# Kernel tuning notes

Hardware: AMD Instinct MI355X
Metric: run time of the kernel (lower is better)

## Reference

```python
import jax, jax.numpy as jnp
import numpy as np

N = 125000   # lattice cells (50^3)
K = 26       # max neighbors (3D Moore neighborhood)
D = 32       # state_size
STEPS = 3    # CNF integration steps (explicit Euler)


def setup_inputs() -> dict:
    key = jax.random.key(0)
    ks = jax.random.split(key, 12)
    s = 0.1  # small init so tanh stays in its linear-ish regime
    return {
        "full_lattice_states": jax.random.normal(ks[0], (N, D), jnp.float32),
        "neighbor_indices": jax.random.randint(ks[1], (N, K), 0, N, jnp.int32),
        "tier_ids": jax.random.randint(ks[2], (N, K), 0, 3, jnp.int32),
        # local expert (SimpleLinear): [cur ; local_agg] -> D
        "W_loc": jax.random.normal(ks[3], (2 * D, D), jnp.float32) * s,
        "b_loc": jnp.zeros((D,), jnp.float32),
        # functional expert (HybridGNN): per-neighbor message + combine
        "W_msg": jax.random.normal(ks[4], (D, D), jnp.float32) * s,
        "b_msg": jnp.zeros((D,), jnp.float32),
        "W_fun": jax.random.normal(ks[5], (2 * D, D), jnp.float32) * s,
        "b_fun": jnp.zeros((D,), jnp.float32),
        # distant expert (LightweightCNF): ODE drift on [x ; distant_agg]
        "W_cnf": jax.random.normal(ks[6], (2 * D, D), jnp.float32) * s,
        "b_cnf": jnp.zeros((D,), jnp.float32),
        # gating network: [cur ; local_agg ; func_agg ; dist_agg] -> 3 experts
        "W_gate": jax.random.normal(ks[7], (4 * D, 3), jnp.float32) * s,
        "b_gate": jnp.zeros((3,), jnp.float32),
    }


def reference(full_lattice_states, neighbor_indices, tier_ids,
              W_loc, b_loc, W_msg, b_msg, W_fun, b_fun,
              W_cnf, b_cnf, W_gate, b_gate):
    cur = full_lattice_states                      # [N, D]
    nbr = full_lattice_states[neighbor_indices]    # [N, K, D] gather (irregular access)

    def tier_mean(x, t):
        # masked mean over neighbors belonging to tier t
        m = (tier_ids == t)[..., None].astype(x.dtype)           # [N, K, 1]
        return (x * m).sum(axis=1) / jnp.maximum(m.sum(axis=1), 1.0)  # [N, D]

    local_agg = tier_mean(nbr, 0)   # [N, D]
    func_agg = tier_mean(nbr, 1)    # [N, D]
    dist_agg = tier_mean(nbr, 2)    # [N, D]

    # local expert: single linear on [cur ; local_agg]
    local_out = jnp.tanh(jnp.concatenate([cur, local_agg], -1) @ W_loc + b_loc)

    # functional expert: GNN message passing over functional-tier neighbors
    msgs = jnp.tanh(nbr @ W_msg + b_msg)           # [N, K, D]
    func_msg = tier_mean(msgs, 1)                  # [N, D]
    func_out = jnp.tanh(jnp.concatenate([cur, func_msg], -1) @ W_fun + b_fun)

    # distant expert: lightweight CNF, explicit Euler conditioned on dist_agg
    dt = 1.0 / STEPS
    x = cur
    for _ in range(STEPS):
        x = x + dt * jnp.tanh(jnp.concatenate([x, dist_agg], -1) @ W_cnf + b_cnf)
    dist_out = x

    # gating: adaptive weighting of the 3 experts
    gate_in = jnp.concatenate([cur, local_agg, func_agg, dist_agg], -1)  # [N, 4D]
    w = jax.nn.softmax(gate_in @ W_gate + b_gate, axis=-1)               # [N, 3]

    out = (w[:, 0:1] * local_out + w[:, 1:2] * func_out + w[:, 2:3] * dist_out)
    return out
```

## Files before the change

kernel.cpp:

```cpp
#include <hip/hip_runtime.h>
#include <hip/hip_bf16.h>
#include <math.h>

#define NCELL 125000
#define KNBR  26
#define D     32
#define MC    64

#define SXE (127.0f/7.0f)
#define SXD (7.0f/127.0f)
#define SMD (1.0f/127.0f)

typedef unsigned int uint4v __attribute__((ext_vector_type(4)));
typedef float float4v __attribute__((ext_vector_type(4)));

__device__ __forceinline__ float fast_tanh(float x) {
    float e = __expf(2.0f * x);
    return 1.0f - 2.0f / (e + 1.0f);
}
__device__ __forceinline__ float bf2f(unsigned int h) {
    return __uint_as_float(h << 16);
}
__device__ __forceinline__ unsigned short f2bf(float f) {
    unsigned int u = __float_as_uint(f);
    u += 0x7fffu + ((u >> 16) & 1u);
    return (unsigned short)(u >> 16);
}

__global__ void __launch_bounds__(256) msg_kernel(
    const float* __restrict__ X, const float* __restrict__ Wm,
    const float* __restrict__ bm, unsigned short* __restrict__ XM)
{
    __shared__ float sX[256];
    int t = blockIdx.x * 256 + threadIdx.x;
    float v = X[t];
    sX[threadIdx.x] = v;
    __syncthreads();
    int d = t & 31;
    int base = threadIdx.x & ~31;
    float acc = bm[d];
#pragma unroll
    for (int j = 0; j < D; ++j)
        acc = fmaf(sX[base + j], Wm[j * D + d], acc);
    int xq = __float2int_rn(fminf(fmaxf(v, -7.f), 7.f) * SXE);
    int mq = __float2int_rn(fast_tanh(acc) * 127.0f);
    XM[t] = (unsigned short)(((mq & 0xff) << 8) | (xq & 0xff));
}

__global__ void __launch_bounds__(256) agg_kernel(
    const unsigned short* __restrict__ XM,
    const int* __restrict__ nbr, const int* __restrict__ tier,
    unsigned short* __restrict__ aggs)
{
    __shared__ int sPack[8 * KNBR];
    int tid = threadIdx.x;
    int blockCell = blockIdx.x * 8;
    if (tid < 8 * KNBR) {
        int g = blockCell * KNBR + tid;
        int jj = __builtin_nontemporal_load(&nbr[g]);
        int tt = __builtin_nontemporal_load(&tier[g]);
        sPack[tid] = (jj << 2) | tt;
    }
    __syncthreads();

    int grp = tid >> 5, d = tid & 31;
    int c = blockCell + grp;
    int sAll = 0, s0 = 0, s1 = 0, sm = 0, n0 = 0, n1 = 0;
#pragma unroll
    for (int k = 0; k < KNBR; ++k) {
        int pk = sPack[grp * KNBR + k];
        int tt = pk & 3;
        int j  = pk >> 2;
        unsigned short v = XM[j * D + d];
        int x = (int)(signed char)(v & 0xff);
        int m = (int)(signed char)(v >> 8);
        bool t0 = (tt == 0), t1 = (tt == 1);
        sAll += x;
        s0 += t0 ? x : 0;   n0 += t0;
        s1 += t1 ? x : 0;   n1 += t1;
        sm += t1 ? m : 0;
    }
    int s2 = sAll - s0 - s1;
    float n2 = (float)(KNBR - n0 - n1);
    unsigned short* a = aggs + (size_t)c * 4 * D + d;
    __builtin_nontemporal_store(f2bf((float)s0 * SXD / fmaxf((float)n0, 1.f)), a + 0 * D);
    __builtin_nontemporal_store(f2bf((float)s1 * SXD / fmaxf((float)n1, 1.f)), a + 1 * D);
    __builtin_nontemporal_store(f2bf((float)s2 * SXD / fmaxf(n2, 1.f)),        a + 2 * D);
    __builtin_nontemporal_store(f2bf((float)sm * SMD / fmaxf((float)n1, 1.f)), a + 3 * D);
}

__global__ void __launch_bounds__(256) moe_kernel(
    const float* __restrict__ X, const unsigned int* __restrict__ aggs,
    const float* __restrict__ Wl, const float* __restrict__ bl,
    const float* __restrict__ Wf, const float* __restrict__ bfv,
    const float* __restrict__ Wc, const float* __restrict__ bc,
    const float* __restrict__ Wg, const float* __restrict__ bg,
    float* __restrict__ out)
{
    __shared__ float sX[MC * 32];
    __shared__ unsigned int sA[MC * 64];
    int tid  = threadIdx.x;
    int base = blockIdx.x * MC;
    int cells = NCELL - base; if (cells > MC) cells = MC;

    const float4* gX = (const float4*)(X + (size_t)base * 32);
#pragma unroll
    for (int k = 0; k < 2; ++k) {
        int q4 = tid + k * 256;
        if (q4 * 4 < cells * 32) {
            float4 v = gX[q4];
            int g = q4 * 4, cc = g >> 5, j = g & 31, s = cc & 31;
            sX[cc * 32 + ((j + 0) ^ s)] = v.x;
            sX[cc * 32 + ((j + 1) ^ s)] = v.y;
            sX[cc * 32 + ((j + 2) ^ s)] = v.z;
            sX[cc * 32 + ((j + 3) ^ s)] = v.w;
        }
    }
    const uint4v* gA = (const uint4v*)(aggs + (size_t)base * 64);
#pragma unroll
    for (int k = 0; k < 4; ++k) {
        int q4 = tid + k * 256;
        if (q4 * 4 < cells * 64) {
            uint4v v = __builtin_nontemporal_load(&gA[q4]);
            int g = q4 * 4, cc = g >> 6, p = g & 63, s = cc & 31;
            sA[cc * 64 + ((p + 0) ^ s)] = v.x;
            sA[cc * 64 + ((p + 1) ^ s)] = v.y;
            sA[cc * 64 + ((p + 2) ^ s)] = v.z;
            sA[cc * 64 + ((p + 3) ^ s)] = v.w;
        }
    }
    __syncthreads();

    int role = tid >> 6, cc = tid & 63;
    int s = cc & 31;
    bool act = (cc < cells);
    float res[32];
    float w0 = 0.f, w1 = 0.f, w2 = 0.f;

    if (act && role == 0) {
        float g0 = bg[0], g1 = bg[1], g2 = bg[2];
#pragma unroll 8
        for (int j = 0; j < 32; ++j) {
            float v = sX[cc * 32 + (j ^ s)];
            g0 = fmaf(v, Wg[j*3+0], g0); g1 = fmaf(v, Wg[j*3+1], g1); g2 = fmaf(v, Wg[j*3+2], g2);
        }
#pragma unroll 8
        for (int p = 0; p < 48; ++p) {
            unsigned int dw = sA[cc * 64 + (p ^ s)];
            float vlo = bf2f(dw & 0xffffu), vhi = bf2f(dw >> 16);
            int r = 32 + p * 2;
            g0 = fmaf(vlo, Wg[r*3+0], g0); g1 = fmaf(vlo, Wg[r*3+1], g1); g2 = fmaf(vlo, Wg[r*3+2], g2);
            g0 = fmaf(vhi, Wg[(r+1)*3+0], g0); g1 = fmaf(vhi, Wg[(r+1)*3+1], g1); g2 = fmaf(vhi, Wg[(r+1)*3+2], g2);
        }
        float mx = fmaxf(g0, fmaxf(g1, g2));
        float e0 = __expf(g0 - mx), e1 = __expf(g1 - mx), e2 = __expf(g2 - mx);
        float inv = 1.f / (e0 + e1 + e2);
        w0 = e0 * inv; w1 = e1 * inv; w2 = e2 * inv;
    } else if (act && role == 1) {
        float gc[32], xx[32];
#pragma unroll
        for (int d0 = 0; d0 < 32; ++d0) gc[d0] = bc[d0];
#pragma unroll 4
        for (int p = 0; p < 16; ++p) {
            unsigned int dw = sA[cc * 64 + ((32 + p) ^ s)];
            float vlo = bf2f(dw & 0xffffu), vhi = bf2f(dw >> 16);
            int j = 32 + p * 2;
#pragma unroll
            for (int d0 = 0; d0 < 32; ++d0) gc[d0] = fmaf(vlo, Wc[j * 32 + d0], gc[d0]);
#pragma unroll
            for (int d0 = 0; d0 < 32; ++d0) gc[d0] = fmaf(vhi, Wc[(j + 1) * 32 + d0], gc[d0]);
        }
#pragma unroll
        for (int d0 = 0; d0 < 32; ++d0) xx[d0] = sX[cc * 32 + (d0 ^ s)];
        const float dt = 1.0f / 3.0f;
#pragma unroll 1
        for (int st = 0; st < 3; ++st) {
#pragma unroll
            for (int d0 = 0; d0 < 32; ++d0) res[d0] = gc[d0];
#pragma unroll 8
            for (int j = 0; j < 32; ++j) {
                float v = xx[j];
#pragma unroll
                for (int d0 = 0; d0 < 32; ++d0) res[d0] = fmaf(v, Wc[j * 32 + d0], res[d0]);
            }
#pragma unroll
            for (int d0 = 0; d0 < 32; ++d0) xx[d0] += dt * fast_tanh(res[d0]);
        }
#pragma unroll
        for (int d0 = 0; d0 < 32; ++d0) res[d0] = xx[d0];
    } else if (act && role == 2) {
#pragma unroll
        for (int d0 = 0; d0 < 32; ++d0) res[d0] = bl[d0];
#pragma unroll 8
        for (int j = 0; j < 32; ++j) {
            float v = sX[cc * 32 + (j ^ s)];
#pragma unroll
            for (int d0 = 0; d0 < 32; ++d0) res[d0] = fmaf(v, Wl[j * 32 + d0], res[d0]);
        }
#pragma unroll 4
        for (int p = 0; p < 16; ++p) {
            unsigned int dw = sA[cc * 64 + (p ^ s)];
            float vlo = bf2f(dw & 0xffffu), vhi = bf2f(dw >> 16);
            int j = 32 + p * 2;
#pragma unroll
            for (int d0 = 0; d0 < 32; ++d0) res[d0] = fmaf(vlo, Wl[j * 32 + d0], res[d0]);
#pragma unroll
            for (int d0 = 0; d0 < 32; ++d0) res[d0] = fmaf(vhi, Wl[(j + 1) * 32 + d0], res[d0]);
        }
#pragma unroll
        for (int d0 = 0; d0 < 32; ++d0) res[d0] = fast_tanh(res[d0]);
    } else if (act && role == 3) {
#pragma unroll
        for (int d0 = 0; d0 < 32; ++d0) res[d0] = bfv[d0];
#pragma unroll 8
        for (int j = 0; j < 32; ++j) {
            float v = sX[cc * 32 + (j ^ s)];
#pragma unroll
            for (int d0 = 0; d0 < 32; ++d0) res[d0] = fmaf(v, Wf[j * 32 + d0], res[d0]);
        }
#pragma unroll 4
        for (int p = 0; p < 16; ++p) {
            unsigned int dw = sA[cc * 64 + ((48 + p) ^ s)];
            float vlo = bf2f(dw & 0xffffu), vhi = bf2f(dw >> 16);
            int j = 32 + p * 2;
#pragma unroll
            for (int d0 = 0; d0 < 32; ++d0) res[d0] = fmaf(vlo, Wf[j * 32 + d0], res[d0]);
#pragma unroll
            for (int d0 = 0; d0 < 32; ++d0) res[d0] = fmaf(vhi, Wf[(j + 1) * 32 + d0], res[d0]);
        }
#pragma unroll
        for (int d0 = 0; d0 < 32; ++d0) res[d0] = fast_tanh(res[d0]);
    }
    __syncthreads();

    float* sFr = (float*)sA;
    float* sCr = sFr + MC * 32;
    if (act) {
        if (role == 2) {
#pragma unroll
            for (int d0 = 0; d0 < 32; ++d0) sX[cc * 32 + (d0 ^ s)] = res[d0];
        } else if (role == 3) {
#pragma unroll
            for (int d0 = 0; d0 < 32; ++d0) sFr[cc * 32 + (d0 ^ s)] = res[d0];
        } else if (role == 1) {
#pragma unroll
            for (int d0 = 0; d0 < 32; ++d0) sCr[cc * 32 + (d0 ^ s)] = res[d0];
        }
    }
    __syncthreads();

    if (act && role == 0) {
        float o[32];
#pragma unroll
        for (int d0 = 0; d0 < 32; ++d0) {
            float lo = sX [cc * 32 + (d0 ^ s)];
            float fo = sFr[cc * 32 + (d0 ^ s)];
            float xo = sCr[cc * 32 + (d0 ^ s)];
            o[d0] = w0 * lo + w1 * fo + w2 * xo;
        }
#pragma unroll
        for (int d0 = 0; d0 < 32; ++d0) sX[cc * 32 + (d0 ^ s)] = o[d0];
    }
    __syncthreads();

    float4v* gO = (float4v*)(out + (size_t)base * 32);
#pragma unroll
    for (int k = 0; k < 2; ++k) {
        int q4 = tid + k * 256;
        if (q4 * 4 < cells * 32) {
            int g = q4 * 4, cc2 = g >> 5, j = g & 31, s2 = cc2 & 31;
            float4v v;
            v.x = sX[cc2 * 32 + ((j + 0) ^ s2)];
            v.y = sX[cc2 * 32 + ((j + 1) ^ s2)];
            v.z = sX[cc2 * 32 + ((j + 2) ^ s2)];
            v.w = sX[cc2 * 32 + ((j + 3) ^ s2)];
            __builtin_nontemporal_store(v, &gO[q4]);
        }
    }
}

extern "C" void kernel_launch(void* const* d_in, const int* in_sizes, int n_in,
                              void* d_out, int out_size, void* d_ws, size_t ws_size,
                              hipStream_t stream)
{
    const float* X    = (const float*)d_in[0];
    const int*   nbr  = (const int*)  d_in[1];
    const int*   tier = (const int*)  d_in[2];
    const float* Wl   = (const float*)d_in[3];
    const float* bl   = (const float*)d_in[4];
    const float* Wm   = (const float*)d_in[5];
    const float* bm   = (const float*)d_in[6];
    const float* Wf   = (const float*)d_in[7];
    const float* bf   = (const float*)d_in[8];
    const float* Wc   = (const float*)d_in[9];
    const float* bc   = (const float*)d_in[10];
    const float* Wg   = (const float*)d_in[11];
    const float* bg   = (const float*)d_in[12];
    float* out = (float*)d_out;

    const size_t ND = (size_t)NCELL * D;
    unsigned short* XM = (unsigned short*)d_ws;
    unsigned short* aggs = XM + ND;

    dim3 blk(256);
    msg_kernel<<<dim3(ND / 256), blk, 0, stream>>>(X, Wm, bm, XM);
    agg_kernel<<<dim3(NCELL / 8), blk, 0, stream>>>(XM, nbr, tier, aggs);
    moe_kernel<<<dim3((NCELL + MC - 1) / MC), blk, 0, stream>>>(
        X, (const unsigned int*)aggs, Wl, bl, Wf, bf, Wc, bc, Wg, bg, out);
}
```

Before: 226.5 us.

## Fuse neighbor aggregation into MoE kernel via shared-memory aggregates

```diff
diff --git a/kernel.cpp b/kernel.cpp
--- a/kernel.cpp
+++ b/kernel.cpp
@@ -11,7 +11,6 @@
 #define SXD (7.0f/127.0f)
 #define SMD (1.0f/127.0f)
 
-typedef unsigned int uint4v __attribute__((ext_vector_type(4)));
 typedef float float4v __attribute__((ext_vector_type(4)));
 
 __device__ __forceinline__ float fast_tanh(float x) {
@@ -47,50 +46,9 @@
     XM[t] = (unsigned short)(((mq & 0xff) << 8) | (xq & 0xff));
 }
 
-__global__ void __launch_bounds__(256) agg_kernel(
-    const unsigned short* __restrict__ XM,
+__global__ void __launch_bounds__(256) fused_kernel(
+    const float* __restrict__ X, const unsigned short* __restrict__ XM,
     const int* __restrict__ nbr, const int* __restrict__ tier,
-    unsigned short* __restrict__ aggs)
-{
-    __shared__ int sPack[8 * KNBR];
-    int tid = threadIdx.x;
-    int blockCell = blockIdx.x * 8;
-    if (tid < 8 * KNBR) {
-        int g = blockCell * KNBR + tid;
-        int jj = __builtin_nontemporal_load(&nbr[g]);
-        int tt = __builtin_nontemporal_load(&tier[g]);
-        sPack[tid] = (jj << 2) | tt;
-    }
-    __syncthreads();
-
-    int grp = tid >> 5, d = tid & 31;
-    int c = blockCell + grp;
-    int sAll = 0, s0 = 0, s1 = 0, sm = 0, n0 = 0, n1 = 0;
-#pragma unroll
-    for (int k = 0; k < KNBR; ++k) {
-        int pk = sPack[grp * KNBR + k];
-        int tt = pk & 3;
-        int j  = pk >> 2;
-        unsigned short v = XM[j * D + d];
-        int x = (int)(signed char)(v & 0xff);
-        int m = (int)(signed char)(v >> 8);
-        bool t0 = (tt == 0), t1 = (tt == 1);
-        sAll += x;
-        s0 += t0 ? x : 0;   n0 += t0;
-        s1 += t1 ? x : 0;   n1 += t1;
-        sm += t1 ? m : 0;
-    }
-    int s2 = sAll - s0 - s1;
-    float n2 = (float)(KNBR - n0 - n1);
-    unsigned short* a = aggs + (size_t)c * 4 * D + d;
-    __builtin_nontemporal_store(f2bf((float)s0 * SXD / fmaxf((float)n0, 1.f)), a + 0 * D);
-    __builtin_nontemporal_store(f2bf((float)s1 * SXD / fmaxf((float)n1, 1.f)), a + 1 * D);
-    __builtin_nontemporal_store(f2bf((float)s2 * SXD / fmaxf(n2, 1.f)),        a + 2 * D);
-    __builtin_nontemporal_store(f2bf((float)sm * SMD / fmaxf((float)n1, 1.f)), a + 3 * D);
-}
-
-__global__ void __launch_bounds__(256) moe_kernel(
-    const float* __restrict__ X, const unsigned int* __restrict__ aggs,
     const float* __restrict__ Wl, const float* __restrict__ bl,
     const float* __restrict__ Wf, const float* __restrict__ bfv,
     const float* __restrict__ Wc, const float* __restrict__ bc,
@@ -99,10 +57,18 @@
 {
     __shared__ float sX[MC * 32];
     __shared__ unsigned int sA[MC * 64];
+    __shared__ int sPack[MC * KNBR];
+    unsigned short* sA16 = (unsigned short*)sA;
+
     int tid  = threadIdx.x;
     int base = blockIdx.x * MC;
     int cells = NCELL - base; if (cells > MC) cells = MC;
 
+    for (int i = tid; i < cells * KNBR; i += 256) {
+        int jj = __builtin_nontemporal_load(&nbr[base * KNBR + i]);
+        int tt = __builtin_nontemporal_load(&tier[base * KNBR + i]);
+        sPack[i] = (jj << 2) | tt;
+    }
     const float4* gX = (const float4*)(X + (size_t)base * 32);
 #pragma unroll
     for (int k = 0; k < 2; ++k) {
@@ -116,17 +82,36 @@
             sX[cc * 32 + ((j + 3) ^ s)] = v.w;
         }
     }
-    const uint4v* gA = (const uint4v*)(aggs + (size_t)base * 64);
-#pragma unroll
-    for (int k = 0; k < 4; ++k) {
-        int q4 = tid + k * 256;
-        if (q4 * 4 < cells * 64) {
-            uint4v v = __builtin_nontemporal_load(&gA[q4]);
-            int g = q4 * 4, cc = g >> 6, p = g & 63, s = cc & 31;
-            sA[cc * 64 + ((p + 0) ^ s)] = v.x;
-            sA[cc * 64 + ((p + 1) ^ s)] = v.y;
-            sA[cc * 64 + ((p + 2) ^ s)] = v.z;
-            sA[cc * 64 + ((p + 3) ^ s)] = v.w;
+    __syncthreads();
+
+    int grp = tid >> 5, d = tid & 31;
+#pragma unroll 1
+    for (int slot = grp; slot < MC; slot += 8) {
+        if (slot < cells) {
+            int sAll = 0, s0 = 0, s1 = 0, sm = 0, n0 = 0, n1 = 0;
+#pragma unroll
+            for (int k = 0; k < KNBR; ++k) {
+                int pk = sPack[slot * KNBR + k];
+                int tt = pk & 3;
+                int j  = pk >> 2;
+                unsigned short v = XM[j * D + d];
+                int x = (int)(signed char)(v & 0xff);
+                int m = (int)(signed char)(v >> 8);
+                bool t0 = (tt == 0), t1 = (tt == 1);
+                sAll += x;
+                s0 += t0 ? x : 0;   n0 += t0;
+                s1 += t1 ? x : 0;   n1 += t1;
+                sm += t1 ? m : 0;
+            }
+            int s2 = sAll - s0 - s1;
+            float n2 = (float)(KNBR - n0 - n1);
+            int s = slot & 31;
+            int b16 = slot * 128;
+            int p = d >> 1, h = d & 1;
+            sA16[b16 + ((( 0 + p) ^ s) << 1) + h] = f2bf((float)s0 * SXD / fmaxf((float)n0, 1.f));
+            sA16[b16 + (((16 + p) ^ s) << 1) + h] = f2bf((float)s1 * SXD / fmaxf((float)n1, 1.f));
+            sA16[b16 + (((32 + p) ^ s) << 1) + h] = f2bf((float)s2 * SXD / fmaxf(n2, 1.f));
+            sA16[b16 + (((48 + p) ^ s) << 1) + h] = f2bf((float)sm * SMD / fmaxf((float)n1, 1.f));
         }
     }
     __syncthreads();
@@ -300,11 +285,9 @@
 
     const size_t ND = (size_t)NCELL * D;
     unsigned short* XM = (unsigned short*)d_ws;
-    unsigned short* aggs = XM + ND;
 
     dim3 blk(256);
     msg_kernel<<<dim3(ND / 256), blk, 0, stream>>>(X, Wm, bm, XM);
-    agg_kernel<<<dim3(NCELL / 8), blk, 0, stream>>>(XM, nbr, tier, aggs);
-    moe_kernel<<<dim3((NCELL + MC - 1) / MC), blk, 0, stream>>>(
-        X, (const unsigned int*)aggs, Wl, bl, Wf, bf, Wc, bc, Wg, bg, out);
-}
+    fused_kernel<<<dim3((NCELL + MC - 1) / MC), blk, 0, stream>>>(
+        X, XM, nbr, tier, Wl, bl, Wf, bf, Wc, bc, Wg, bg, out);
+}
```

Result: no change. 222.6 us (-1.7%).
